# Performance work log

Hardware: AMD Instinct MI355X
Metric: run time of the kernel (lower is better)

Reference implementation:

```python
import jax, jax.numpy as jnp
import numpy as np
from jax import lax

B = 8; SEQ = 512; NVAR = 1024; PRED = 96; TFEAT = 7
DM = 128; DSTATE = 16; DCONV = 2; EL = 2; DFF = 128
DIN = DM                      # expand = 1
DTR = (DM + 15) // 16         # dt_rank = ceil(d_model/16) = 8


def setup_inputs() -> dict:
    key = jax.random.key(0)
    ks = iter(jax.random.split(key, 40))
    def rn(shape, s=0.02):
        return jax.random.normal(next(ks), shape, jnp.float32) * s
    inp = {}
    inp["x_enc"] = jax.random.normal(next(ks), (B, SEQ, NVAR), jnp.float32)
    inp["x_mark_enc"] = jax.random.normal(next(ks), (B, SEQ, TFEAT), jnp.float32)
    inp["x_dec"] = jnp.zeros((1, 1, 1), jnp.float32)
    inp["x_mark_dec"] = jnp.zeros((1, 1, 1), jnp.float32)
    # inverted embedding: Linear(seq_len -> d_model)
    inp["emb_w"] = rn((DM, SEQ)); inp["emb_b"] = jnp.zeros((DM,), jnp.float32)
    # Mamba params, stacked [e_layers, 2 directions, ...]
    inp["in_proj_w"] = rn((EL, 2, 2 * DIN, DM))
    inp["conv_w"] = rn((EL, 2, DIN, DCONV), 0.5)
    inp["conv_b"] = jnp.zeros((EL, 2, DIN), jnp.float32)
    inp["x_proj_w"] = rn((EL, 2, DTR + 2 * DSTATE, DIN))
    inp["dt_proj_w"] = rn((EL, 2, DIN, DTR), 0.5)
    inp["dt_proj_b"] = rn((EL, 2, DIN), 0.1)
    A_init = jnp.log(jnp.tile(jnp.arange(1, DSTATE + 1, dtype=jnp.float32), (DIN, 1)))
    inp["A_log"] = jnp.broadcast_to(A_init, (EL, 2, DIN, DSTATE)) * 1.0
    inp["D_param"] = jnp.ones((EL, 2, DIN), jnp.float32)
    inp["out_proj_w"] = rn((EL, 2, DM, DIN))
    # EncoderLayer norms + pointwise FFN (conv1/conv2 with kernel 1)
    inp["norm1_w"] = jnp.ones((EL, DM), jnp.float32); inp["norm1_b"] = jnp.zeros((EL, DM), jnp.float32)
    inp["norm2_w"] = jnp.ones((EL, DM), jnp.float32); inp["norm2_b"] = jnp.zeros((EL, DM), jnp.float32)
    inp["ffn_w1"] = rn((EL, DFF, DM)); inp["ffn_b1"] = jnp.zeros((EL, DFF), jnp.float32)
    inp["ffn_w2"] = rn((EL, DM, DFF)); inp["ffn_b2"] = jnp.zeros((EL, DM), jnp.float32)
    inp["fnorm_w"] = jnp.ones((DM,), jnp.float32); inp["fnorm_b"] = jnp.zeros((DM,), jnp.float32)
    inp["proj_w"] = rn((PRED, DM)); inp["proj_b"] = jnp.zeros((PRED,), jnp.float32)
    return inp


def _layernorm(x, w, b):
    mu = x.mean(-1, keepdims=True)
    var = ((x - mu) ** 2).mean(-1, keepdims=True)
    return (x - mu) / jnp.sqrt(var + 1e-5) * w + b


def _mamba(x, ipw, cw, cb, xpw, dpw, dpb, A_log, Dp, opw):
    # x: [B, L, DM]
    Bb, L, _ = x.shape
    xz = x @ ipw.T                                  # [B,L,2*DIN]
    xr, z = xz[..., :DIN], xz[..., DIN:]
    # causal depthwise conv1d, kernel DCONV, padding DCONV-1, truncated to L
    xp = jnp.pad(xr, ((0, 0), (DCONV - 1, 0), (0, 0)))
    xc = sum(xp[:, k:k + L, :] * cw[:, k] for k in range(DCONV)) + cb
    xc = jax.nn.silu(xc)
    dbc = xc @ xpw.T                                # [B,L,DTR+2*DSTATE]
    dt = dbc[..., :DTR]
    Bm = dbc[..., DTR:DTR + DSTATE]
    Cm = dbc[..., DTR + DSTATE:]
    delta = jax.nn.softplus(dt @ dpw.T + dpb)       # [B,L,DIN]
    A = -jnp.exp(A_log)                             # [DIN,DSTATE]
    dA = jnp.exp(delta[..., None] * A)              # [B,L,DIN,DSTATE]
    dBu = delta[..., None] * Bm[:, :, None, :] * xc[..., None]

    def step(h, t):
        dA_t, dBu_t, C_t = t
        h = dA_t * h + dBu_t                        # [B,DIN,DSTATE]
        y = jnp.einsum('bdn,bn->bd', h, C_t)
        return h, y

    h0 = jnp.zeros((Bb, DIN, DSTATE), x.dtype)
    _, ys = lax.scan(step, h0, (dA.transpose(1, 0, 2, 3), dBu.transpose(1, 0, 2, 3), Cm.transpose(1, 0, 2)))
    y = ys.transpose(1, 0, 2) + Dp * xc             # [B,L,DIN]
    y = y * jax.nn.silu(z)
    return y @ opw.T


def reference(x_enc, x_mark_enc, x_dec, x_mark_dec, emb_w, emb_b, in_proj_w, conv_w, conv_b,
              x_proj_w, dt_proj_w, dt_proj_b, A_log, D_param, out_proj_w,
              norm1_w, norm1_b, norm2_w, norm2_b, ffn_w1, ffn_b1, ffn_w2, ffn_b2,
              fnorm_w, fnorm_b, proj_w, proj_b):
    N = x_enc.shape[-1]
    x = jnp.where(x_enc == -9999.0, -1.0, x_enc)
    # inverted embedding: variate tokens + 7 time-feature tokens
    tokens = jnp.concatenate([x.transpose(0, 2, 1), x_mark_enc.transpose(0, 2, 1)], axis=1)  # [B,N+7,SEQ]
    h = tokens @ emb_w.T + emb_b                    # [B,N+7,DM]
    for l in range(EL):
        fwd = _mamba(h, in_proj_w[l, 0], conv_w[l, 0], conv_b[l, 0], x_proj_w[l, 0],
                     dt_proj_w[l, 0], dt_proj_b[l, 0], A_log[l, 0], D_param[l, 0], out_proj_w[l, 0])
        rev = _mamba(h[:, ::-1], in_proj_w[l, 1], conv_w[l, 1], conv_b[l, 1], x_proj_w[l, 1],
                     dt_proj_w[l, 1], dt_proj_b[l, 1], A_log[l, 1], D_param[l, 1], out_proj_w[l, 1])[:, ::-1]
        h = h + fwd + rev
        y = h = _layernorm(h, norm1_w[l], norm1_b[l])
        y = jax.nn.relu(y @ ffn_w1[l].T + ffn_b1[l])
        y = y @ ffn_w2[l].T + ffn_b2[l]
        h = _layernorm(h + y, norm2_w[l], norm2_b[l])
    h = _layernorm(h, fnorm_w, fnorm_b)
    dec = (h @ proj_w.T + proj_b).transpose(0, 2, 1)[:, :, :N]  # [B,PRED,N]
    return dec[:, -PRED:, :]
```

## Files before the change

### kernel.cpp

```cpp
#include <hip/hip_runtime.h>
#include <math.h>


#define L_SEQ 1031
#define LP    1152
#define TC    36
#define NCH   32
#define SDROW 1056
#define BATCH 8
#define NVAR  1024
#define SEQQ  512
#define TFEAT 7

#define SZ_H    ((size_t)BATCH * L_SEQ * 128)
#define SZ_XZ   ((size_t)2 * BATCH * L_SEQ * 256)
#define SZ_DT   ((size_t)2 * BATCH * 128 * LP)
#define SZ_BC   ((size_t)2 * BATCH * 16 * LP)
#define OFF_H    ((size_t)0)
#define OFF_H1   (OFF_H + SZ_H)
#define OFF_XZ   (OFF_H1 + SZ_H)
#define OFF_XCT  (OFF_XZ + SZ_XZ)
#define OFF_DLT  (OFF_XCT + SZ_DT)
#define OFF_BMT  (OFF_DLT + SZ_DT)
#define OFF_CMT  (OFF_BMT + SZ_BC)
#define OFF_YT   (OFF_CMT + SZ_BC)
#define SZ_SUM  ((size_t)2 * BATCH * NCH * 128 * 16)

typedef __bf16 bf16_t;
typedef bf16_t bf16x4 __attribute__((ext_vector_type(4)));
typedef bf16_t bf16x8 __attribute__((ext_vector_type(8)));
typedef float floatx4 __attribute__((ext_vector_type(4)));

#define MFMA16(a, b, c) __builtin_amdgcn_mfma_f32_16x16x32_bf16((a), (b), (c), 0, 0, 0)

__device__ __forceinline__ float silu_f(float x) {
  return x / (1.f + __expf(-x));
}
__device__ __forceinline__ float softplus_f(float x) {
  return (x > 20.f) ? x : log1pf(__expf(x));
}
__device__ __forceinline__ float red8(float x) {
  x += __int_as_float(__builtin_amdgcn_update_dpp(
      0, __float_as_int(x), 0xB1, 0xF, 0xF, true));
  x += __int_as_float(__builtin_amdgcn_update_dpp(
      0, __float_as_int(x), 0x4E, 0xF, 0xF, true));
  x += __int_as_float(__builtin_amdgcn_update_dpp(
      0, __float_as_int(x), 0x141, 0xF, 0xF, true));
  return x;
}

#define STAGE_W128(WBUF, SRC, LDK, K0)                                       \
  _Pragma("unroll")                                                          \
  for (int i_ = 0; i_ < 16; i_++) {                                          \
    int e_ = tid + i_ * 256;                                                 \
    int n_ = e_ >> 5, kq_ = e_ & 31;                                         \
    float4 wv_ = *(const float4*)&(SRC)[(size_t)n_ * (LDK) + (K0) + kq_ * 4];\
    bf16x4 bv_ = {(bf16_t)wv_.x, (bf16_t)wv_.y, (bf16_t)wv_.z, (bf16_t)wv_.w};\
    *(bf16x4*)&WBUF[n_][kq_ * 4] = bv_;                                      \
  }

#define MFMA_K128(ABUF, WBUF, ACC)                                           \
  _Pragma("unroll")                                                          \
  for (int kc_ = 0; kc_ < 4; kc_++) {                                        \
    bf16x8 a_ = *(const bf16x8*)&ABUF[arow][kc_ * 32 + q8];                  \
    _Pragma("unroll")                                                        \
    for (int nt_ = 0; nt_ < 4; nt_++) {                                      \
      bf16x8 b_ = *(const bf16x8*)&WBUF[wcol + nt_ * 16 + ln][kc_ * 32 + q8];\
      ACC[nt_] = MFMA16(a_, b_, ACC[nt_]);                                   \
    }                                                                        \
  }

__global__ __launch_bounds__(256) void k_embed(
    const float* __restrict__ x_enc, const float* __restrict__ x_mark,
    const float* __restrict__ emb_w, const float* __restrict__ emb_b,
    float* __restrict__ H) {
  int b = blockIdx.y;
  int v0 = blockIdx.x * 32;
  int tid = threadIdx.x;
  __shared__ bf16_t Abf[32][136];
  __shared__ bf16_t Wbf[128][136];
  int lane = tid & 63, ln = lane & 15, q = lane >> 4, q8 = q * 8;
  int w = tid >> 6, rw = w & 1, cw = w >> 1;
  int arow = rw * 16 + ln, wcol = cw * 64;
  floatx4 acc[4];
#pragma unroll
  for (int nt = 0; nt < 4; nt++) acc[nt] = (floatx4){0.f, 0.f, 0.f, 0.f};

  for (int c = 0; c < 4; c++) {
    int s0 = c * 128;
#pragma unroll
    for (int i = 0; i < 4; i++) {
      int e = tid + i * 256;
      int s = e >> 3, vq = e & 7;
      int vg = v0 + vq * 4;
      float4 xv;
      if (vg + 3 < NVAR) {
        xv = *(const float4*)&x_enc[((size_t)b * SEQQ + s0 + s) * NVAR + vg];
        if (xv.x == -9999.f) xv.x = -1.f;
        if (xv.y == -9999.f) xv.y = -1.f;
        if (xv.z == -9999.f) xv.z = -1.f;
        if (xv.w == -9999.f) xv.w = -1.f;
      } else {
        float tmp[4];
#pragma unroll
        for (int u = 0; u < 4; u++) {
          int v = vg + u;
          tmp[u] = (v < L_SEQ)
                       ? x_mark[((size_t)b * SEQQ + s0 + s) * TFEAT + (v - NVAR)]
                       : 0.f;
        }
        xv = make_float4(tmp[0], tmp[1], tmp[2], tmp[3]);
      }
      Abf[vq * 4 + 0][s] = (bf16_t)xv.x;
      Abf[vq * 4 + 1][s] = (bf16_t)xv.y;
      Abf[vq * 4 + 2][s] = (bf16_t)xv.z;
      Abf[vq * 4 + 3][s] = (bf16_t)xv.w;
    }
    STAGE_W128(Wbf, emb_w, SEQQ, s0);
    __syncthreads();
    MFMA_K128(Abf, Wbf, acc);
    __syncthreads();
  }
#pragma unroll
  for (int r = 0; r < 4; r++) {
    int v = v0 + rw * 16 + q * 4 + r;
    if (v < L_SEQ) {
      float* dst = &H[((size_t)b * L_SEQ + v) * 128];
#pragma unroll
      for (int nt = 0; nt < 4; nt++) {
        int col = wcol + nt * 16 + ln;
        dst[col] = acc[nt][r] + emb_b[col];
      }
    }
  }
}

__global__ __launch_bounds__(256) void k_xz(
    const float* __restrict__ H, const float* __restrict__ ipw,
    float* __restrict__ XZ, int l) {
  int b = blockIdx.y;
  int dir = blockIdx.z >> 1, nh = blockIdx.z & 1;
  int t0 = blockIdx.x * 32;
  int tid = threadIdx.x;
  __shared__ bf16_t Abf[32][136];
  __shared__ bf16_t Wbf[128][136];
  int lane = tid & 63, ln = lane & 15, q = lane >> 4, q8 = q * 8;
  int w = tid >> 6, rw = w & 1, cw = w >> 1;
  int arow = rw * 16 + ln, wcol = cw * 64;
  floatx4 acc[4];
#pragma unroll
  for (int nt = 0; nt < 4; nt++) acc[nt] = (floatx4){0.f, 0.f, 0.f, 0.f};
  const float* wbase = ipw + (size_t)(l * 2 + dir) * 256 * 128 + (size_t)nh * 128 * 128;

#pragma unroll
  for (int i = 0; i < 4; i++) {
    int e = tid + i * 256;
    int tl = e >> 5, kq = e & 31;
    int t = t0 + tl;
    float4 hv = make_float4(0.f, 0.f, 0.f, 0.f);
    if (t < L_SEQ) {
      int st = dir ? (L_SEQ - 1 - t) : t;
      hv = *(const float4*)&H[((size_t)b * L_SEQ + st) * 128 + kq * 4];
    }
    bf16x4 av = {(bf16_t)hv.x, (bf16_t)hv.y, (bf16_t)hv.z, (bf16_t)hv.w};
    *(bf16x4*)&Abf[tl][kq * 4] = av;
  }
  STAGE_W128(Wbf, wbase, 128, 0);
  __syncthreads();
  MFMA_K128(Abf, Wbf, acc);

#pragma unroll
  for (int r = 0; r < 4; r++) {
    int t = t0 + rw * 16 + q * 4 + r;
    if (t < L_SEQ) {
      float* dst = XZ + ((size_t)(dir * BATCH + b) * L_SEQ + t) * 256 + nh * 128;
#pragma unroll
      for (int nt = 0; nt < 4; nt++) dst[wcol + nt * 16 + ln] = acc[nt][r];
    }
  }
}

__global__ __launch_bounds__(256) void k_mid(
    const float* __restrict__ XZ,
    const float* __restrict__ conv_w, const float* __restrict__ conv_b,
    const float* __restrict__ xpw,
    const float* __restrict__ dpw, const float* __restrict__ dpb,
    float* __restrict__ XCT, float* __restrict__ DLT,
    float* __restrict__ BmT, float* __restrict__ CmT, int l) {
  int b = blockIdx.y, dir = blockIdx.z;
  int t0 = blockIdx.x * 32;
  int tid = threadIdx.x;
  int pg = l * 2 + dir;
  __shared__ float xcs[32][132];
  __shared__ float xpws[40][128];
  __shared__ float dbcs[40][36];
  const float* xz = XZ + (size_t)(dir * BATCH + b) * L_SEQ * 256;

  for (int i = 0; i < 20; i++) {
    int e = tid + i * 256;
    int k = e & 127, j = e >> 7;
    xpws[j][k] = xpw[((size_t)pg * 40 + j) * 128 + k];
  }
  for (int i = 0; i < 16; i++) {
    int e = tid + i * 256;
    int d = e & 127, tl = e >> 7;
    int t = t0 + tl;
    float v = 0.f;
    if (t < L_SEQ) {
      float x1 = xz[(size_t)t * 256 + d];
      float x0 = (t > 0) ? xz[(size_t)(t - 1) * 256 + d] : 0.f;
      float c0 = conv_w[((size_t)pg * 128 + d) * 2 + 0];
      float c1 = conv_w[((size_t)pg * 128 + d) * 2 + 1];
      v = silu_f(x0 * c0 + x1 * c1 + conv_b[(size_t)pg * 128 + d]);
    }
    xcs[tl][d] = v;
  }
  __syncthreads();
  {
    int tl = tid & 31, jg = tid >> 5;
    float acc[5] = {0.f};
    const float4* xrow = (const float4*)&xcs[tl][0];
    for (int kk = 0; kk < 32; kk++) {
      float4 a = xrow[kk];
#pragma unroll
      for (int jj = 0; jj < 5; jj++) {
        float4 w = ((const float4*)&xpws[jg * 5 + jj][0])[kk];
        acc[jj] = fmaf(a.x, w.x, acc[jj]);
        acc[jj] = fmaf(a.y, w.y, acc[jj]);
        acc[jj] = fmaf(a.z, w.z, acc[jj]);
        acc[jj] = fmaf(a.w, w.w, acc[jj]);
      }
    }
#pragma unroll
    for (int jj = 0; jj < 5; jj++) dbcs[jg * 5 + jj][tl] = acc[jj];
  }
  __syncthreads();
  for (int i = 0; i < 4; i++) {
    int e = tid + i * 256;
    int tl = e & 31, r = e >> 5;
    int n = r & 15, isC = r >> 4;
    int t = t0 + tl;
    if (t < LP) {
      float v = dbcs[8 + isC * 16 + n][tl];
      float* dst = isC ? CmT : BmT;
      dst[((size_t)(dir * BATCH + b) * 16 + n) * LP + t] = v;
    }
  }
  {
    int d = tid & 127, th = tid >> 7;
    float dw[8];
#pragma unroll
    for (int k = 0; k < 8; k++) dw[k] = dpw[((size_t)pg * 128 + d) * 8 + k];
    float dbv = dpb[(size_t)pg * 128 + d];
    size_t base = ((size_t)(dir * BATCH + b) * 128 + d) * LP;
    for (int tb = th * 16; tb < th * 16 + 16; tb += 4) {
      int t = t0 + tb;
      if (t < LP) {
        float dv[4], xv[4];
#pragma unroll
        for (int u = 0; u < 4; u++) {
          int tl = tb + u;
          float a = dbv;
#pragma unroll
          for (int k = 0; k < 8; k++) a = fmaf(dbcs[k][tl], dw[k], a);
          dv[u] = softplus_f(a);
          xv[u] = xcs[tl][d];
        }
        *(float4*)(DLT + base + t) = make_float4(dv[0], dv[1], dv[2], dv[3]);
        *(float4*)(XCT + base + t) = make_float4(xv[0], xv[1], xv[2], xv[3]);
      }
    }
  }
}

__global__ __launch_bounds__(64) void k_scan1(
    const float* __restrict__ DLT, const float* __restrict__ XCT,
    const float* __restrict__ BmT,
    const float* __restrict__ A_log,
    float* __restrict__ sumH, float* __restrict__ YT, int l) {
  int z = blockIdx.z;
  int dir = z >> 5, j = z & 31;
  int b = blockIdx.y;
  int lane = threadIdx.x;
  int np = lane & 7, ds = lane >> 3;
  int d = blockIdx.x * 8 + ds;
  int pg = l * 2 + dir;
  int n0 = np * 2;
  int dirb = dir * BATCH + b;
  float A0 = -__expf(A_log[((size_t)pg * 128 + d) * 16 + n0]);
  float A1 = -__expf(A_log[((size_t)pg * 128 + d) * 16 + n0 + 1]);
  size_t bd = ((size_t)dirb * 128 + d) * LP + (size_t)j * TC;
  size_t bn = ((size_t)dirb * 16 + n0) * LP + (size_t)j * TC;
  const float4* dl4 = (const float4*)(DLT + bd);
  const float4* xc4 = (const float4*)(XCT + bd);
  const float4* b04 = (const float4*)(BmT + bn);
  const float4* b14 = (const float4*)(BmT + bn + LP);
  float h0 = 0.f, h1 = 0.f, sdl = 0.f;
  const int NI = TC / 4;
  float4 cd = dl4[0], cx = xc4[0], cb0 = b04[0], cb1 = b14[0];
#define P1STEP(DL, XC, B0, B1)                       \
  {                                                  \
    float du_ = (DL) * (XC);                         \
    h0 = fmaf(__expf((DL) * A0), h0, du_ * (B0));    \
    h1 = fmaf(__expf((DL) * A1), h1, du_ * (B1));    \
  }
  for (int i = 0; i < NI; i++) {
    float4 nd = cd, nx = cx, nb0 = cb0, nb1 = cb1;
    if (i + 1 < NI) {
      nd = dl4[i + 1]; nx = xc4[i + 1];
      nb0 = b04[i + 1]; nb1 = b14[i + 1];
    }
    P1STEP(cd.x, cx.x, cb0.x, cb1.x);
    P1STEP(cd.y, cx.y, cb0.y, cb1.y);
    P1STEP(cd.z, cx.z, cb0.z, cb1.z);
    P1STEP(cd.w, cx.w, cb0.w, cb1.w);
    sdl += (cd.x + cd.y) + (cd.z + cd.w);
    cd = nd; cx = nx; cb0 = nb0; cb1 = nb1;
  }
#undef P1STEP
  size_t si = (((size_t)dirb * NCH + j) * 128 + d) * 16 + n0;
  *(float2*)&sumH[si] = make_float2(h0, h1);
  if (np == 0) {
    YT[((size_t)dirb * LP + SDROW + j) * 128 + d] = sdl;
  }
}

__global__ __launch_bounds__(64) void k_scan2(
    const float* __restrict__ DLT, const float* __restrict__ XCT,
    const float* __restrict__ BmT, const float* __restrict__ CmT,
    const float* __restrict__ XZ,
    const float* __restrict__ A_log, const float* __restrict__ Dpar,
    const float* __restrict__ sumH,
    float* __restrict__ YT, int l) {
  int z = blockIdx.z;
  int dir = z >> 5, j = z & 31;
  int b = blockIdx.y;
  int lane = threadIdx.x;
  int np = lane & 7, ds = lane >> 3;
  int d = blockIdx.x * 8 + ds;
  int pg = l * 2 + dir;
  int n0 = np * 2;
  int dirb = dir * BATCH + b;
  float A0 = -__expf(A_log[((size_t)pg * 128 + d) * 16 + n0]);
  float A1 = -__expf(A_log[((size_t)pg * 128 + d) * 16 + n0 + 1]);
  float Dv = Dpar[(size_t)pg * 128 + d];
  float h0 = 0.f, h1 = 0.f;
  {
    size_t sbase = ((size_t)dirb * NCH) * 2048 + (size_t)d * 16 + n0;
    const float* sdbase = YT + ((size_t)dirb * LP + SDROW) * 128 + d;
    for (int jj = 0; jj < j; jj++) {
      float2 hE = *(const float2*)&sumH[sbase + (size_t)jj * 2048];
      float sdl = sdbase[(size_t)jj * 128];
      h0 = fmaf(__expf(A0 * sdl), h0, hE.x);
      h1 = fmaf(__expf(A1 * sdl), h1, hE.y);
    }
  }
  size_t bd = ((size_t)dirb * 128 + d) * LP + (size_t)j * TC;
  size_t bn = ((size_t)dirb * 16 + n0) * LP + (size_t)j * TC;
  const float4* dl4 = (const float4*)(DLT + bd);
  const float4* xc4 = (const float4*)(XCT + bd);
  const float4* b04 = (const float4*)(BmT + bn);
  const float4* b14 = (const float4*)(BmT + bn + LP);
  const float4* c04 = (const float4*)(CmT + bn);
  const float4* c14 = (const float4*)(CmT + bn + LP);
  const float* zbase = XZ + (size_t)dirb * L_SEQ * 256 + 128 + d
                       + (size_t)j * TC * 256;
  float* ybase = YT + ((size_t)dirb * LP + (size_t)j * TC) * 128 + d;
  const int NI = TC / 4;
  float4 cd = dl4[0], cx = xc4[0], cb0 = b04[0], cb1 = b14[0];
  float4 cc0 = c04[0], cc1 = c14[0];
  float zc[4], zn[4];
  if (np == 0) {
#pragma unroll
    for (int u = 0; u < 4; u++) zc[u] = zbase[(size_t)u * 256];
  }
#define STEP1(DL, XC, B0, B1, C0, C1, YO)            \
  {                                                  \
    float du_ = (DL) * (XC);                         \
    h0 = fmaf(__expf((DL) * A0), h0, du_ * (B0));    \
    h1 = fmaf(__expf((DL) * A1), h1, du_ * (B1));    \
    float p_ = red8(fmaf(h1, (C1), h0 * (C0)));      \
    (YO) = fmaf(Dv, (XC), p_);                       \
  }
  for (int i = 0; i < NI; i++) {
    float4 nd = cd, nx = cx, nb0 = cb0, nb1 = cb1, nc0 = cc0, nc1 = cc1;
    if (i + 1 < NI) {
      nd = dl4[i + 1]; nx = xc4[i + 1];
      nb0 = b04[i + 1]; nb1 = b14[i + 1];
      nc0 = c04[i + 1]; nc1 = c14[i + 1];
      if (np == 0) {
        int tb = (i + 1) * 4;
#pragma unroll
        for (int u = 0; u < 4; u++) zn[u] = zbase[(size_t)(tb + u) * 256];
      }
    }
    float4 y;
    STEP1(cd.x, cx.x, cb0.x, cb1.x, cc0.x, cc1.x, y.x);
    STEP1(cd.y, cx.y, cb0.y, cb1.y, cc0.y, cc1.y, y.y);
    STEP1(cd.z, cx.z, cb0.z, cb1.z, cc0.z, cc1.z, y.z);
    STEP1(cd.w, cx.w, cb0.w, cb1.w, cc0.w, cc1.w, y.w);
    if (np == 0) {
      int tg = j * TC + i * 4;
      float yv[4] = {y.x * silu_f(zc[0]), y.y * silu_f(zc[1]),
                     y.z * silu_f(zc[2]), y.w * silu_f(zc[3])};
#pragma unroll
      for (int u = 0; u < 4; u++) {
        if (tg + u < SDROW) ybase[(size_t)(i * 4 + u) * 128] = yv[u];
      }
#pragma unroll
      for (int u = 0; u < 4; u++) zc[u] = zn[u];
    }
    cd = nd; cx = nx; cb0 = nb0; cb1 = nb1; cc0 = nc0; cc1 = nc1;
  }
#undef STEP1
}

__global__ __launch_bounds__(256) void k_out(
    const float* __restrict__ YT, const float* __restrict__ Hin,
    const float* __restrict__ opw,
    const float* __restrict__ n1w, const float* __restrict__ n1b,
    float* __restrict__ H1, int l) {
  int b = blockIdx.y;
  int t0 = blockIdx.x * 32;
  int tid = threadIdx.x;
  __shared__ bf16_t Abf[32][136];
  __shared__ bf16_t Wbf[128][136];
  __shared__ float Ssum[2][32][2];
  int lane = tid & 63, ln = lane & 15, q = lane >> 4, q8 = q * 8;
  int w = tid >> 6, rw = w & 1, cw = w >> 1;
  int arow = rw * 16 + ln, wcol = cw * 64;
  floatx4 acc[4];
#pragma unroll
  for (int nt = 0; nt < 4; nt++) acc[nt] = (floatx4){0.f, 0.f, 0.f, 0.f};

  for (int dirp = 0; dirp < 2; dirp++) {
    const float* ysrc = YT + (size_t)(dirp * BATCH + b) * LP * 128;
#pragma unroll
    for (int i = 0; i < 4; i++) {
      int e = tid + i * 256;
      int tl = e >> 5, dq = e & 31;
      int tg = t0 + tl;
      int srow = dirp ? (L_SEQ - 1 - tg) : tg;
      float4 yv = make_float4(0.f, 0.f, 0.f, 0.f);
      if (srow >= 0) yv = *(const float4*)&ysrc[(size_t)srow * 128 + dq * 4];
      bf16x4 av = {(bf16_t)yv.x, (bf16_t)yv.y, (bf16_t)yv.z, (bf16_t)yv.w};
      *(bf16x4*)&Abf[tl][dq * 4] = av;
    }
    const float* wsrc = opw + (size_t)(l * 2 + dirp) * 128 * 128;
    STAGE_W128(Wbf, wsrc, 128, 0);
    __syncthreads();
    MFMA_K128(Abf, Wbf, acc);
    __syncthreads();
  }
  const float* nw = n1w + l * 128;
  const float* nbv = n1b + l * 128;
  float vres[4][4];
  float s1r[4], s2r[4];
#pragma unroll
  for (int r = 0; r < 4; r++) {
    int t = t0 + rw * 16 + q * 4 + r;
    float s1 = 0.f, s2 = 0.f;
#pragma unroll
    for (int nt = 0; nt < 4; nt++) {
      int col = wcol + nt * 16 + ln;
      float resid = (t < L_SEQ) ? Hin[((size_t)b * L_SEQ + t) * 128 + col] : 0.f;
      float v = acc[nt][r] + resid;
      vres[r][nt] = v;
      s1 += v;
      s2 += v * v;
    }
#pragma unroll
    for (int m = 1; m < 16; m <<= 1) {
      s1 += __shfl_xor(s1, m);
      s2 += __shfl_xor(s2, m);
    }
    s1r[r] = s1; s2r[r] = s2;
  }
  if (ln == 0) {
#pragma unroll
    for (int r = 0; r < 4; r++) {
      Ssum[cw][rw * 16 + q * 4 + r][0] = s1r[r];
      Ssum[cw][rw * 16 + q * 4 + r][1] = s2r[r];
    }
  }
  __syncthreads();
#pragma unroll
  for (int r = 0; r < 4; r++) {
    int row = rw * 16 + q * 4 + r;
    float s1 = s1r[r] + Ssum[cw ^ 1][row][0];
    float s2 = s2r[r] + Ssum[cw ^ 1][row][1];
    float mean = s1 * (1.f / 128.f);
    float rstd = rsqrtf(s2 * (1.f / 128.f) - mean * mean + 1e-5f);
    int t = t0 + row;
    if (t < L_SEQ) {
#pragma unroll
      for (int nt = 0; nt < 4; nt++) {
        int col = wcol + nt * 16 + ln;
        H1[((size_t)b * L_SEQ + t) * 128 + col] =
            (vres[r][nt] - mean) * rstd * nw[col] + nbv[col];
      }
    }
  }
}

__global__ __launch_bounds__(256) void k_ffn(
    const float* __restrict__ H1, const float* __restrict__ w1,
    const float* __restrict__ b1, const float* __restrict__ w2,
    const float* __restrict__ b2, const float* __restrict__ n2w,
    const float* __restrict__ n2b, float* __restrict__ Hout, int l) {
  int b = blockIdx.y;
  int t0 = blockIdx.x * 32;
  int tid = threadIdx.x;
  __shared__ bf16_t Abf[32][136];
  __shared__ bf16_t Wbf[128][136];
  __shared__ bf16_t Ut[32][136];
  __shared__ float Ssum[2][32][2];
  int lane = tid & 63, ln = lane & 15, q = lane >> 4, q8 = q * 8;
  int w = tid >> 6, rw = w & 1, cw = w >> 1;
  int arow = rw * 16 + ln, wcol = cw * 64;
  floatx4 acc[4];
#pragma unroll
  for (int nt = 0; nt < 4; nt++) acc[nt] = (floatx4){0.f, 0.f, 0.f, 0.f};
  const float* w1b = w1 + (size_t)l * 128 * 128;
  const float* w2b = w2 + (size_t)l * 128 * 128;

#pragma unroll
  for (int i = 0; i < 4; i++) {
    int e = tid + i * 256;
    int tl = e >> 5, kq = e & 31;
    int t = t0 + tl;
    float4 hv = make_float4(0.f, 0.f, 0.f, 0.f);
    if (t < L_SEQ)
      hv = *(const float4*)&H1[((size_t)b * L_SEQ + t) * 128 + kq * 4];
    bf16x4 av = {(bf16_t)hv.x, (bf16_t)hv.y, (bf16_t)hv.z, (bf16_t)hv.w};
    *(bf16x4*)&Abf[tl][kq * 4] = av;
  }
  STAGE_W128(Wbf, w1b, 128, 0);
  __syncthreads();
  MFMA_K128(Abf, Wbf, acc);
  __syncthreads();
  {
    float b1v[4];
#pragma unroll
    for (int nt = 0; nt < 4; nt++) b1v[nt] = b1[l * 128 + wcol + nt * 16 + ln];
#pragma unroll
    for (int nt = 0; nt < 4; nt++) {
#pragma unroll
      for (int r = 0; r < 4; r++) {
        Ut[rw * 16 + q * 4 + r][wcol + nt * 16 + ln] =
            (bf16_t)fmaxf(acc[nt][r] + b1v[nt], 0.f);
      }
      acc[nt] = (floatx4){0.f, 0.f, 0.f, 0.f};
    }
  }
  STAGE_W128(Wbf, w2b, 128, 0);
  __syncthreads();
  MFMA_K128(Ut, Wbf, acc);
  const float* nw = n2w + l * 128;
  const float* nbv = n2b + l * 128;
  float vres[4][4];
  float s1r[4], s2r[4];
#pragma unroll
  for (int r = 0; r < 4; r++) {
    int t = t0 + rw * 16 + q * 4 + r;
    float s1 = 0.f, s2 = 0.f;
#pragma unroll
    for (int nt = 0; nt < 4; nt++) {
      int col = wcol + nt * 16 + ln;
      float resid = (t < L_SEQ) ? H1[((size_t)b * L_SEQ + t) * 128 + col] : 0.f;
      float v = acc[nt][r] + b2[l * 128 + col] + resid;
      vres[r][nt] = v;
      s1 += v;
      s2 += v * v;
    }
#pragma unroll
    for (int m = 1; m < 16; m <<= 1) {
      s1 += __shfl_xor(s1, m);
      s2 += __shfl_xor(s2, m);
    }
    s1r[r] = s1; s2r[r] = s2;
  }
  __syncthreads();
  if (ln == 0) {
#pragma unroll
    for (int r = 0; r < 4; r++) {
      Ssum[cw][rw * 16 + q * 4 + r][0] = s1r[r];
      Ssum[cw][rw * 16 + q * 4 + r][1] = s2r[r];
    }
  }
  __syncthreads();
#pragma unroll
  for (int r = 0; r < 4; r++) {
    int row = rw * 16 + q * 4 + r;
    float s1 = s1r[r] + Ssum[cw ^ 1][row][0];
    float s2 = s2r[r] + Ssum[cw ^ 1][row][1];
    float mean = s1 * (1.f / 128.f);
    float rstd = rsqrtf(s2 * (1.f / 128.f) - mean * mean + 1e-5f);
    int t = t0 + row;
    if (t < L_SEQ) {
#pragma unroll
      for (int nt = 0; nt < 4; nt++) {
        int col = wcol + nt * 16 + ln;
        Hout[((size_t)b * L_SEQ + t) * 128 + col] =
            (vres[r][nt] - mean) * rstd * nw[col] + nbv[col];
      }
    }
  }
}

__global__ __launch_bounds__(256) void k_final(
    const float* __restrict__ Hsrc, const float* __restrict__ fw,
    const float* __restrict__ fb, const float* __restrict__ pw,
    const float* __restrict__ pb, float* __restrict__ out) {
  int b = blockIdx.y;
  int v0 = blockIdx.x * 16;
  int tid = threadIdx.x;
  __shared__ float At[128][17];
  __shared__ float Ws[32][97];
  __shared__ float Os[96][17];
  for (int i = 0; i < 8; i++) {
    int e = tid + i * 256;
    int k = e & 127, tl = e >> 7;
    At[k][tl] = Hsrc[((size_t)b * L_SEQ + v0 + tl) * 128 + k];
  }
  __syncthreads();
  {
    int g = tid & 15, tl = tid >> 4;
    float s1 = 0.f, s2 = 0.f;
#pragma unroll
    for (int kk = 0; kk < 8; kk++) {
      float v = At[g * 8 + kk][tl];
      s1 += v;
      s2 += v * v;
    }
#pragma unroll
    for (int msk = 1; msk < 16; msk <<= 1) {
      s1 += __shfl_xor(s1, msk);
      s2 += __shfl_xor(s2, msk);
    }
    float mean = s1 * (1.f / 128.f);
    float rstd = rsqrtf(s2 * (1.f / 128.f) - mean * mean + 1e-5f);
#pragma unroll
    for (int kk = 0; kk < 8; kk++) {
      int k = g * 8 + kk;
      At[k][tl] = (At[k][tl] - mean) * rstd * fw[k] + fb[k];
    }
  }
  __syncthreads();
  int tm = tid & 15, tt = tid >> 4;
  float acc[6] = {0.f};
  for (int k0 = 0; k0 < 128; k0 += 32) {
    for (int i = 0; i < 12; i++) {
      int e = tid + i * 256;
      int ki = e & 31, p = e >> 5;
      Ws[ki][p] = pw[(size_t)p * 128 + k0 + ki];
    }
    __syncthreads();
    for (int ki = 0; ki < 32; ki++) {
      float a = At[k0 + ki][tt];
#pragma unroll
      for (int jq = 0; jq < 6; jq++)
        acc[jq] = fmaf(a, Ws[ki][tm + jq * 16], acc[jq]);
    }
    __syncthreads();
  }
#pragma unroll
  for (int jq = 0; jq < 6; jq++) {
    int p = tm + jq * 16;
    Os[p][tt] = acc[jq] + pb[p];
  }
  __syncthreads();
  for (int i = 0; i < 6; i++) {
    int e = tid + i * 256;
    int vi = e & 15, p = e >> 4;
    out[((size_t)b * 96 + p) * 1024 + v0 + vi] = Os[p][vi];
  }
}

extern "C" void kernel_launch(void* const* d_in, const int* in_sizes, int n_in,
                              void* d_out, int out_size, void* d_ws, size_t ws_size,
                              hipStream_t stream) {
  (void)in_sizes; (void)n_in; (void)out_size; (void)ws_size;
  const float* x_enc  = (const float*)d_in[0];
  const float* x_mark = (const float*)d_in[1];
  const float* emb_w  = (const float*)d_in[4];
  const float* emb_b  = (const float*)d_in[5];
  const float* ipw    = (const float*)d_in[6];
  const float* cw     = (const float*)d_in[7];
  const float* cb     = (const float*)d_in[8];
  const float* xpw    = (const float*)d_in[9];
  const float* dpw    = (const float*)d_in[10];
  const float* dpb    = (const float*)d_in[11];
  const float* A_log  = (const float*)d_in[12];
  const float* Dpar   = (const float*)d_in[13];
  const float* opw    = (const float*)d_in[14];
  const float* n1w    = (const float*)d_in[15];
  const float* n1b    = (const float*)d_in[16];
  const float* n2w    = (const float*)d_in[17];
  const float* n2b    = (const float*)d_in[18];
  const float* fw1    = (const float*)d_in[19];
  const float* fb1    = (const float*)d_in[20];
  const float* fw2    = (const float*)d_in[21];
  const float* fb2    = (const float*)d_in[22];
  const float* fnw    = (const float*)d_in[23];
  const float* fnb    = (const float*)d_in[24];
  const float* pw     = (const float*)d_in[25];
  const float* pb     = (const float*)d_in[26];

  float* ws   = (float*)d_ws;
  float* H    = ws + OFF_H;
  float* H1   = ws + OFF_H1;
  float* XZ   = ws + OFF_XZ;
  float* XCT  = ws + OFF_XCT;
  float* DLT  = ws + OFF_DLT;
  float* BmT  = ws + OFF_BMT;
  float* CmT  = ws + OFF_CMT;
  float* YT   = ws + OFF_YT;
  float* sumH = ws + OFF_H1;

  k_embed<<<dim3(33, 8), 256, 0, stream>>>(x_enc, x_mark, emb_w, emb_b, H);
  for (int l = 0; l < 2; l++) {
    k_xz<<<dim3(33, 8, 4), 256, 0, stream>>>(H, ipw, XZ, l);
    k_mid<<<dim3(36, 8, 2), 256, 0, stream>>>(XZ, cw, cb, xpw, dpw, dpb,
                                              XCT, DLT, BmT, CmT, l);
    k_scan1<<<dim3(16, 8, 64), 64, 0, stream>>>(DLT, XCT, BmT, A_log,
                                                sumH, YT, l);
    k_scan2<<<dim3(16, 8, 64), 64, 0, stream>>>(DLT, XCT, BmT, CmT, XZ,
                                                A_log, Dpar, sumH, YT, l);
    k_out<<<dim3(33, 8), 256, 0, stream>>>(YT, H, opw, n1w, n1b, H1, l);
    k_ffn<<<dim3(33, 8), 256, 0, stream>>>(H1, fw1, fb1, fw2, fb2, n2w, n2b, H, l);
  }
  k_final<<<dim3(64, 8), 256, 0, stream>>>(H, fnw, fnb, pw, pb, (float*)d_out);
}
```

Baseline: 417.5 us.

## Add separate inter-chunk prefix scan kernel and pack 4 chunks per block

The chunked selective scan previously had each chunk in k_scan2 recompute the carry-in state by looping over all earlier chunk summaries, which is quadratic in chunk count. A new k_scanp kernel does one sequential prefix pass over the 32 chunk summaries per (dir,batch,d,n) and writes the exclusive prefix state back into sumH in place. k_scan2 then just loads its starting state. Scan kernels are also widened to 256-thread blocks holding 4 chunks each. This adds one extra kernel launch and a small serial kernel with low parallelism.

```diff
diff --git a/kernel.cpp b/kernel.cpp
--- a/kernel.cpp
+++ b/kernel.cpp
@@ -273,15 +273,18 @@
   }
 }
 
-__global__ __launch_bounds__(64) void k_scan1(
+__global__ __launch_bounds__(256) void k_scan1(
     const float* __restrict__ DLT, const float* __restrict__ XCT,
     const float* __restrict__ BmT,
     const float* __restrict__ A_log,
     float* __restrict__ sumH, float* __restrict__ YT, int l) {
+  int tid = threadIdx.x;
+  int wid = tid >> 6;
+  int lane = tid & 63;
   int z = blockIdx.z;
-  int dir = z >> 5, j = z & 31;
+  int dir = z >> 3, jg = z & 7;
+  int j = jg * 4 + wid;
   int b = blockIdx.y;
-  int lane = threadIdx.x;
   int np = lane & 7, ds = lane >> 3;
   int d = blockIdx.x * 8 + ds;
   int pg = l * 2 + dir;
@@ -325,16 +328,10 @@
   }
 }
 
-__global__ __launch_bounds__(64) void k_scan2(
-    const float* __restrict__ DLT, const float* __restrict__ XCT,
-    const float* __restrict__ BmT, const float* __restrict__ CmT,
-    const float* __restrict__ XZ,
-    const float* __restrict__ A_log, const float* __restrict__ Dpar,
-    const float* __restrict__ sumH,
-    float* __restrict__ YT, int l) {
-  int z = blockIdx.z;
-  int dir = z >> 5, j = z & 31;
-  int b = blockIdx.y;
+__global__ __launch_bounds__(64) void k_scanp(
+    const float* __restrict__ A_log, float* __restrict__ sumH,
+    const float* __restrict__ YT, int l) {
+  int dir = blockIdx.z, b = blockIdx.y;
   int lane = threadIdx.x;
   int np = lane & 7, ds = lane >> 3;
   int d = blockIdx.x * 8 + ds;
@@ -343,18 +340,50 @@
   int dirb = dir * BATCH + b;
   float A0 = -__expf(A_log[((size_t)pg * 128 + d) * 16 + n0]);
   float A1 = -__expf(A_log[((size_t)pg * 128 + d) * 16 + n0 + 1]);
+  size_t sbase = (((size_t)dirb * NCH) * 128 + d) * 16 + n0;
+  const float* sdbase = YT + ((size_t)dirb * LP + SDROW) * 128 + d;
+  float h0 = 0.f, h1 = 0.f;
+  float2 hE = *(const float2*)&sumH[sbase];
+  float sdl = sdbase[0];
+  for (int j = 0; j < NCH; j++) {
+    float2 hEn;
+    float sdln;
+    if (j + 1 < NCH) {
+      hEn = *(const float2*)&sumH[sbase + (size_t)(j + 1) * 2048];
+      sdln = sdbase[(size_t)(j + 1) * 128];
+    }
+    *(float2*)&sumH[sbase + (size_t)j * 2048] = make_float2(h0, h1);
+    h0 = fmaf(__expf(A0 * sdl), h0, hE.x);
+    h1 = fmaf(__expf(A1 * sdl), h1, hE.y);
+    hE = hEn;
+    sdl = sdln;
+  }
+}
+
+__global__ __launch_bounds__(256) void k_scan2(
+    const float* __restrict__ DLT, const float* __restrict__ XCT,
+    const float* __restrict__ BmT, const float* __restrict__ CmT,
+    const float* __restrict__ XZ,
+    const float* __restrict__ A_log, const float* __restrict__ Dpar,
+    const float* __restrict__ sumH,
+    float* __restrict__ YT, int l) {
+  int tid = threadIdx.x;
+  int wid = tid >> 6;
+  int lane = tid & 63;
+  int z = blockIdx.z;
+  int dir = z >> 3, jg = z & 7;
+  int j = jg * 4 + wid;
+  int b = blockIdx.y;
+  int np = lane & 7, ds = lane >> 3;
+  int d = blockIdx.x * 8 + ds;
+  int pg = l * 2 + dir;
+  int n0 = np * 2;
+  int dirb = dir * BATCH + b;
+  float A0 = -__expf(A_log[((size_t)pg * 128 + d) * 16 + n0]);
+  float A1 = -__expf(A_log[((size_t)pg * 128 + d) * 16 + n0 + 1]);
   float Dv = Dpar[(size_t)pg * 128 + d];
-  float h0 = 0.f, h1 = 0.f;
-  {
-    size_t sbase = ((size_t)dirb * NCH) * 2048 + (size_t)d * 16 + n0;
-    const float* sdbase = YT + ((size_t)dirb * LP + SDROW) * 128 + d;
-    for (int jj = 0; jj < j; jj++) {
-      float2 hE = *(const float2*)&sumH[sbase + (size_t)jj * 2048];
-      float sdl = sdbase[(size_t)jj * 128];
-      h0 = fmaf(__expf(A0 * sdl), h0, hE.x);
-      h1 = fmaf(__expf(A1 * sdl), h1, hE.y);
-    }
-  }
+  float2 hi = *(const float2*)&sumH[(((size_t)dirb * NCH + j) * 128 + d) * 16 + n0];
+  float h0 = hi.x, h1 = hi.y;
   size_t bd = ((size_t)dirb * 128 + d) * LP + (size_t)j * TC;
   size_t bn = ((size_t)dirb * 16 + n0) * LP + (size_t)j * TC;
   const float4* dl4 = (const float4*)(DLT + bd);
@@ -723,10 +752,11 @@
     k_xz<<<dim3(33, 8, 4), 256, 0, stream>>>(H, ipw, XZ, l);
     k_mid<<<dim3(36, 8, 2), 256, 0, stream>>>(XZ, cw, cb, xpw, dpw, dpb,
                                               XCT, DLT, BmT, CmT, l);
-    k_scan1<<<dim3(16, 8, 64), 64, 0, stream>>>(DLT, XCT, BmT, A_log,
-                                                sumH, YT, l);
-    k_scan2<<<dim3(16, 8, 64), 64, 0, stream>>>(DLT, XCT, BmT, CmT, XZ,
-                                                A_log, Dpar, sumH, YT, l);
+    k_scan1<<<dim3(16, 8, 16), 256, 0, stream>>>(DLT, XCT, BmT, A_log,
+                                                 sumH, YT, l);
+    k_scanp<<<dim3(16, 8, 2), 64, 0, stream>>>(A_log, sumH, YT, l);
+    k_scan2<<<dim3(16, 8, 16), 256, 0, stream>>>(DLT, XCT, BmT, CmT, XZ,
+                                                 A_log, Dpar, sumH, YT, l);
     k_out<<<dim3(33, 8), 256, 0, stream>>>(YT, H, opw, n1w, n1b, H1, l);
     k_ffn<<<dim3(33, 8), 256, 0, stream>>>(H1, fw1, fb1, fw2, fb2, n2w, n2b, H, l);
   }
```

Measured after the change: 407.7 us. 2.3% less time.
